# Kernel tuning notes

Hardware: AMD Instinct MI355X
Metric: run time of the kernel (lower is better)

Reference implementation:

```python
import jax, jax.numpy as jnp
import numpy as np

N = 200_000        # nodes
E = 2_000_000      # edges (before self loops)
D = 128            # emb_dim
L = 5              # num_layer
NUM_ATOM = 120     # num_atom_type
NUM_CHI = 3        # num_chirality_tag
NUM_BOND = 6       # num_bond_type
NUM_DIR = 3        # num_bond_direction
EPS = 1e-5


def setup_inputs() -> dict:
    key = jax.random.key(0)
    ks = jax.random.split(key, 12)
    s = 0.1
    return {
        "x": jax.random.randint(ks[0], (N, 2), 0, 3, dtype=jnp.int64) if jax.config.jax_enable_x64 else jax.random.randint(ks[0], (N, 2), 0, 3, dtype=jnp.int32),
        "edge_index": jax.random.randint(ks[1], (2, E), 0, N, dtype=jnp.int32),
        "edge_attr": jax.random.randint(ks[2], (E, 2), 0, 3, dtype=jnp.int32),
        "x_emb1": jax.random.normal(ks[3], (NUM_ATOM, D), jnp.float32) * s,
        "x_emb2": jax.random.normal(ks[4], (NUM_CHI, D), jnp.float32) * s,
        "edge_emb1": jax.random.normal(ks[5], (L, NUM_BOND, D), jnp.float32) * s,
        "edge_emb2": jax.random.normal(ks[6], (L, NUM_DIR, D), jnp.float32) * s,
        "w1": jax.random.normal(ks[7], (L, D, 2 * D), jnp.float32) * s,
        "b1": jnp.zeros((L, 2 * D), jnp.float32),
        "w2": jax.random.normal(ks[8], (L, 2 * D, D), jnp.float32) * s,
        "b2": jnp.zeros((L, D), jnp.float32),
        "bn_gamma": jnp.ones((L, D), jnp.float32),
        "bn_beta": jnp.zeros((L, D), jnp.float32),
    }


def reference(x, edge_index, edge_attr, x_emb1, x_emb2, edge_emb1, edge_emb2,
              w1, b1, w2, b2, bn_gamma, bn_beta):
    # node features: atom-type emb + chirality emb
    h = x_emb1[x[:, 0]] + x_emb2[x[:, 1]]                     # [N, D]

    # add self loops; self-loop edge_attr = [4, 0]
    loop = jnp.arange(N, dtype=edge_index.dtype)
    src = jnp.concatenate([edge_index[0], loop])              # [E+N]
    dst = jnp.concatenate([edge_index[1], loop])              # [E+N]
    ea0 = jnp.concatenate([edge_attr[:, 0], jnp.full((N,), 4, edge_attr.dtype)])
    ea1 = jnp.concatenate([edge_attr[:, 1], jnp.zeros((N,), edge_attr.dtype)])

    for l in range(L):
        e_emb = edge_emb1[l][ea0] + edge_emb2[l][ea1]         # [E+N, D]
        msg = h[src] + e_emb                                  # gather + add
        agg = jax.ops.segment_sum(msg, dst, num_segments=N)   # scatter-add
        hid = jax.nn.relu(agg @ w1[l] + b1[l])                # [N, 2D]
        hn = hid @ w2[l] + b2[l]                              # [N, D]
        # BatchNorm1d (training mode, biased variance)
        mean = hn.mean(axis=0)
        var = jnp.mean((hn - mean) ** 2, axis=0)
        hn = bn_gamma[l] * (hn - mean) * jax.lax.rsqrt(var + EPS) + bn_beta[l]
        if l < L - 1:
            hn = jax.nn.relu(hn)
        h = hn
    return h
```

## Files before the change

### kernel.cpp

```cpp
#include <hip/hip_runtime.h>

#define NN 200000
#define NPAD 200192
#define NE 2000000
#define DD 128
#define EPSF 1e-5f

typedef short short4v __attribute__((ext_vector_type(4)));
typedef short short8v __attribute__((ext_vector_type(8)));
typedef float f32x4 __attribute__((ext_vector_type(4)));
typedef unsigned long long u64;

__device__ __forceinline__ ushort f2bf(float f) {
  uint u = __float_as_uint(f);
  uint r = u + 0x7fff + ((u >> 16) & 1);
  return (ushort)(r >> 16);
}
__device__ __forceinline__ float bf2f(ushort u) { return __uint_as_float(((uint)u) << 16); }
__device__ __forceinline__ float bflo(uint v) { return __uint_as_float(v << 16); }
__device__ __forceinline__ float bfhi(uint v) { return __uint_as_float(v & 0xffff0000u); }
__device__ __forceinline__ uint packbf(float a, float b) {
  return (uint)f2bf(a) | ((uint)f2bf(b) << 16);
}

__device__ __forceinline__ short8v ldfrag(const ushort* p) {
  short4v lo = *(const short4v*)p;
  short4v hi = *(const short4v*)(p + 16);
  short8v r;
  r[0] = lo[0]; r[1] = lo[1]; r[2] = lo[2]; r[3] = lo[3];
  r[4] = hi[0]; r[5] = hi[1]; r[6] = hi[2]; r[7] = hi[3];
  return r;
}

__global__ __launch_bounds__(256) void k_init(const int* __restrict__ x,
    const float* __restrict__ e1, const float* __restrict__ e2,
    uint* __restrict__ h) {
  int t = blockIdx.x * 256 + threadIdx.x;
  if (t >= NN * 64) return;
  int node = t >> 6, cp = (t & 63) << 1;
  int a = x[2 * node], b = x[2 * node + 1];
  float2 va = *(const float2*)(e1 + (size_t)a * DD + cp);
  float2 vb = *(const float2*)(e2 + (size_t)b * DD + cp);
  h[t] = packbf(va.x + vb.x, va.y + vb.y);
}

__global__ __launch_bounds__(256) void k_cvtw(const float* __restrict__ w,
    ushort* __restrict__ wt, int K, int Nc) {
  int t = blockIdx.x * 256 + threadIdx.x;
  if (t >= 5 * K * Nc) return;
  int per = K * Nc;
  int l = t / per, r0 = t % per;
  int j = r0 & 7, lane = (r0 >> 3) & 63, idx = r0 >> 9;
  int KB = K >> 5;
  int kb = idx % KB, ct = idx / KB;
  int lr = lane & 15, qq = lane >> 4;
  int n = ct * 16 + lr;
  int k = kb * 32 + qq * 4 + (j & 3) + ((j >> 2) << 4);
  wt[t] = f2bf(w[(size_t)l * per + (size_t)k * Nc + n]);
}

__global__ __launch_bounds__(256) void k_hist(const int* __restrict__ ei,
    const int* __restrict__ ea, u64* __restrict__ hist) {
  int e = blockIdx.x * 256 + threadIdx.x;
  if (e >= NE) return;
  int d = ei[NE + e];
  int a0 = ea[2 * e];
  int a1 = ea[2 * e + 1];
  u64 v = (1ull << (a0 * 10)) | (1ull << (30 + a1 * 10));
  atomicAdd(&hist[d], v);
}

__global__ __launch_bounds__(256) void k_scan1(const u64* __restrict__ hist,
    int* __restrict__ off, int* __restrict__ bsum) {
  __shared__ int sh[256];
  int i = blockIdx.x * 256 + threadIdx.x;
  int v = 0;
  if (i < NN) {
    u64 hv = hist[i];
    v = (int)((hv & 1023) + ((hv >> 10) & 1023) + ((hv >> 20) & 1023));
  }
  sh[threadIdx.x] = v;
  __syncthreads();
  for (int d = 1; d < 256; d <<= 1) {
    int xv = 0;
    if (threadIdx.x >= d) xv = sh[threadIdx.x - d];
    __syncthreads();
    if (threadIdx.x >= d) sh[threadIdx.x] += xv;
    __syncthreads();
  }
  if (i < NN) off[i] = sh[threadIdx.x] - v;
  if (threadIdx.x == 255) bsum[blockIdx.x] = sh[255];
}

__global__ __launch_bounds__(1024) void k_scan2(const int* __restrict__ bsum,
    int* __restrict__ boff, int nb) {
  __shared__ int sh[1024];
  int t = threadIdx.x;
  int v = (t < nb) ? bsum[t] : 0;
  sh[t] = v;
  __syncthreads();
  for (int d = 1; d < 1024; d <<= 1) {
    int xv = 0;
    if (t >= d) xv = sh[t - d];
    __syncthreads();
    if (t >= d) sh[t] += xv;
    __syncthreads();
  }
  if (t < nb) boff[t] = sh[t] - v;
}

__global__ __launch_bounds__(256) void k_scan3(int* __restrict__ off,
    const int* __restrict__ boff, int* __restrict__ cursor) {
  int i = blockIdx.x * 256 + threadIdx.x;
  if (i < NN) {
    int o = off[i] + boff[i >> 8];
    off[i] = o;
    cursor[i] = o;
  }
  if (i == 0) off[NN] = NE;
}

__global__ __launch_bounds__(256) void k_scatter(const int* __restrict__ ei,
    int* __restrict__ cursor, int* __restrict__ csr_src) {
  int e = blockIdx.x * 256 + threadIdx.x;
  if (e >= NE) return;
  int d = ei[NE + e];
  int p = atomicAdd(&cursor[d], 1);
  csr_src[p] = ei[e];
}

__global__ __launch_bounds__(256) void k_agg(const uint* __restrict__ h,
    uint* __restrict__ agghi, uint* __restrict__ agglo,
    const int* __restrict__ off, const int* __restrict__ src,
    const u64* __restrict__ hist,
    const float* __restrict__ E1, const float* __restrict__ E2) {
  int lane = threadIdx.x & 63;
  int node = blockIdx.x * 4 + (threadIdx.x >> 6);
  int qq = lane >> 4;
  int c = lane & 15;
  float a[8];
#pragma unroll
  for (int j = 0; j < 8; ++j) a[j] = 0.f;
  int beg = off[node], end = off[node + 1];
  int deg = end - beg;
  for (int base = 0; base < deg; base += 64) {
    int nrem = min(deg - base, 64);
    int myidx = 0;
    if (lane < nrem) myidx = src[beg + base + lane];
    int niter = (nrem + 3) >> 2;
    for (int m = 0; m < niter; m += 2) {
      int slot0 = qq + 4 * m;
      int slot1 = slot0 + 4;
      int s0 = __shfl(myidx, min(slot0, nrem - 1));
      int s1 = __shfl(myidx, min(slot1, nrem - 1));
      uint4 v0 = *(const uint4*)(h + (size_t)s0 * 64 + c * 4);
      if (slot0 < nrem) {
        a[0] += bflo(v0.x); a[1] += bfhi(v0.x);
        a[2] += bflo(v0.y); a[3] += bfhi(v0.y);
        a[4] += bflo(v0.z); a[5] += bfhi(v0.z);
        a[6] += bflo(v0.w); a[7] += bfhi(v0.w);
      }
      if (m + 1 < niter) {
        uint4 v1 = *(const uint4*)(h + (size_t)s1 * 64 + c * 4);
        if (slot1 < nrem) {
          a[0] += bflo(v1.x); a[1] += bfhi(v1.x);
          a[2] += bflo(v1.y); a[3] += bfhi(v1.y);
          a[4] += bflo(v1.z); a[5] += bfhi(v1.z);
          a[6] += bflo(v1.w); a[7] += bfhi(v1.w);
        }
      }
    }
  }
#pragma unroll
  for (int j = 0; j < 8; ++j) {
    a[j] += __shfl_xor(a[j], 16);
    a[j] += __shfl_xor(a[j], 32);
  }
  if (lane < 16) {
    uint4 sv = *(const uint4*)(h + (size_t)node * 64 + c * 4);
    a[0] += bflo(sv.x); a[1] += bfhi(sv.x);
    a[2] += bflo(sv.y); a[3] += bfhi(sv.y);
    a[4] += bflo(sv.z); a[5] += bfhi(sv.z);
    a[6] += bflo(sv.w); a[7] += bfhi(sv.w);
    u64 hv = hist[node];
    float cnt[7] = {
      (float)(int)(hv & 1023),
      (float)(int)((hv >> 10) & 1023),
      (float)(int)((hv >> 20) & 1023),
      1.f,
      (float)(int)((hv >> 30) & 1023) + 1.f,
      (float)(int)((hv >> 40) & 1023),
      (float)(int)((hv >> 50) & 1023)
    };
    const float* rows[7] = {E1, E1 + DD, E1 + 2 * DD, E1 + 4 * DD,
                            E2, E2 + DD, E2 + 2 * DD};
#pragma unroll
    for (int q = 0; q < 7; ++q) {
      f32x4 e0 = *(const f32x4*)(rows[q] + c * 8);
      f32x4 e1v = *(const f32x4*)(rows[q] + c * 8 + 4);
#pragma unroll
      for (int j = 0; j < 4; ++j) { a[j] += cnt[q] * e0[j]; a[4 + j] += cnt[q] * e1v[j]; }
    }
    uint4 hi4, lo4;
    {
      ushort hA, hB;
      hA = f2bf(a[0]); hB = f2bf(a[1]);
      hi4.x = (uint)hA | ((uint)hB << 16);
      lo4.x = (uint)f2bf(a[0] - bf2f(hA)) | ((uint)f2bf(a[1] - bf2f(hB)) << 16);
      hA = f2bf(a[2]); hB = f2bf(a[3]);
      hi4.y = (uint)hA | ((uint)hB << 16);
      lo4.y = (uint)f2bf(a[2] - bf2f(hA)) | ((uint)f2bf(a[3] - bf2f(hB)) << 16);
      hA = f2bf(a[4]); hB = f2bf(a[5]);
      hi4.z = (uint)hA | ((uint)hB << 16);
      lo4.z = (uint)f2bf(a[4] - bf2f(hA)) | ((uint)f2bf(a[5] - bf2f(hB)) << 16);
      hA = f2bf(a[6]); hB = f2bf(a[7]);
      hi4.w = (uint)hA | ((uint)hB << 16);
      lo4.w = (uint)f2bf(a[6] - bf2f(hA)) | ((uint)f2bf(a[7] - bf2f(hB)) << 16);
    }
    *(uint4*)(agghi + (size_t)node * 64 + c * 4) = hi4;
    *(uint4*)(agglo + (size_t)node * 64 + c * 4) = lo4;
  }
}

__global__ __launch_bounds__(512, 1) void k_mlp(
    const ushort* __restrict__ agghi, const ushort* __restrict__ agglo,
    const ushort* __restrict__ w1,
    const float* __restrict__ b1,
    const ushort* __restrict__ w2,
    const float* __restrict__ b2, float* __restrict__ hn,
    float* __restrict__ bnsums) {
  __shared__ uint4 smem4[8192];
  __shared__ float sstat[256];
  const ushort* sw1 = (const ushort*)smem4;
  const ushort* sw2 = (const ushort*)(smem4 + 4096);
  int t = threadIdx.x;
  int lane = t & 63;
  int wid = t >> 6;
  int nb = blockIdx.x * 256 + wid * 32;
  int lr = lane & 15, qq = lane >> 4;

  if (t < 256) sstat[t] = 0.f;

  short8v afh[2][4], afl[2][4];
#pragma unroll
  for (int g = 0; g < 2; ++g) {
    const ushort* ph = agghi + (size_t)(nb + g * 16 + lr) * 128 + qq * 4;
    const ushort* pl = agglo + (size_t)(nb + g * 16 + lr) * 128 + qq * 4;
#pragma unroll
    for (int kb = 0; kb < 4; ++kb) {
      afh[g][kb] = ldfrag(ph + kb * 32);
      afl[g][kb] = ldfrag(pl + kb * 32);
    }
  }

  {
    const uint4* g1 = (const uint4*)w1;
    const uint4* g2 = (const uint4*)w2;
#pragma unroll
    for (int i = 0; i < 8; ++i) smem4[i * 512 + t] = g1[i * 512 + t];
#pragma unroll
    for (int i = 0; i < 8; ++i) smem4[4096 + i * 512 + t] = g2[i * 512 + t];
  }
  __syncthreads();

  f32x4 acc2[2][8];
#pragma unroll
  for (int g = 0; g < 2; ++g)
#pragma unroll
    for (int ct = 0; ct < 8; ++ct) acc2[g][ct] = (f32x4){0.f, 0.f, 0.f, 0.f};

#pragma unroll
  for (int ph = 0; ph < 4; ++ph) {
    f32x4 acc1[2][4];
#pragma unroll
    for (int g = 0; g < 2; ++g)
#pragma unroll
      for (int ct = 0; ct < 4; ++ct) acc1[g][ct] = (f32x4){0.f, 0.f, 0.f, 0.f};
#pragma unroll
    for (int ct = 0; ct < 4; ++ct) {
      int gct = ph * 4 + ct;
#pragma unroll
      for (int kb = 0; kb < 4; ++kb) {
        short8v wf = *(const short8v*)(sw1 + ((gct * 4 + kb) * 64 + lane) * 8);
        acc1[0][ct] = __builtin_amdgcn_mfma_f32_16x16x32_bf16(wf, afh[0][kb], acc1[0][ct], 0, 0, 0);
        acc1[0][ct] = __builtin_amdgcn_mfma_f32_16x16x32_bf16(wf, afl[0][kb], acc1[0][ct], 0, 0, 0);
        acc1[1][ct] = __builtin_amdgcn_mfma_f32_16x16x32_bf16(wf, afh[1][kb], acc1[1][ct], 0, 0, 0);
        acc1[1][ct] = __builtin_amdgcn_mfma_f32_16x16x32_bf16(wf, afl[1][kb], acc1[1][ct], 0, 0, 0);
      }
    }
    short8v hfh[2][2], hfl[2][2];
#pragma unroll
    for (int i = 0; i < 2; ++i) {
      f32x4 ba = *(const f32x4*)(b1 + (ph * 4 + 2 * i) * 16 + qq * 4);
      f32x4 bb = *(const f32x4*)(b1 + (ph * 4 + 2 * i + 1) * 16 + qq * 4);
#pragma unroll
      for (int g = 0; g < 2; ++g) {
        short8v hh, hl;
#pragma unroll
        for (int r = 0; r < 4; ++r) {
          float va = fmaxf(acc1[g][2 * i][r] + ba[r], 0.f);
          float vb = fmaxf(acc1[g][2 * i + 1][r] + bb[r], 0.f);
          ushort ha = f2bf(va), hb = f2bf(vb);
          hh[r] = (short)ha; hh[4 + r] = (short)hb;
          hl[r] = (short)f2bf(va - bf2f(ha));
          hl[4 + r] = (short)f2bf(vb - bf2f(hb));
        }
        hfh[g][i] = hh; hfl[g][i] = hl;
      }
    }
#pragma unroll
    for (int ct = 0; ct < 8; ++ct) {
#pragma unroll
      for (int i = 0; i < 2; ++i) {
        int kb2 = ph * 2 + i;
        short8v wf = *(const short8v*)(sw2 + ((ct * 8 + kb2) * 64 + lane) * 8);
        acc2[0][ct] = __builtin_amdgcn_mfma_f32_16x16x32_bf16(wf, hfh[0][i], acc2[0][ct], 0, 0, 0);
        acc2[0][ct] = __builtin_amdgcn_mfma_f32_16x16x32_bf16(wf, hfl[0][i], acc2[0][ct], 0, 0, 0);
        acc2[1][ct] = __builtin_amdgcn_mfma_f32_16x16x32_bf16(wf, hfh[1][i], acc2[1][ct], 0, 0, 0);
        acc2[1][ct] = __builtin_amdgcn_mfma_f32_16x16x32_bf16(wf, hfl[1][i], acc2[1][ct], 0, 0, 0);
      }
    }
  }

  int n0 = nb + lr, n1 = nb + 16 + lr;
  float m0 = (n0 < NN) ? 1.f : 0.f;
  float m1 = (n1 < NN) ? 1.f : 0.f;
#pragma unroll
  for (int ct = 0; ct < 8; ++ct) {
    f32x4 bb = *(const f32x4*)(b2 + ct * 16 + qq * 4);
    f32x4 o0, o1;
#pragma unroll
    for (int r = 0; r < 4; ++r) {
      o0[r] = acc2[0][ct][r] + bb[r];
      o1[r] = acc2[1][ct][r] + bb[r];
    }
#pragma unroll
    for (int r = 0; r < 4; ++r) {
      float s = m0 * o0[r] + m1 * o1[r];
      float q = m0 * o0[r] * o0[r] + m1 * o1[r] * o1[r];
      s += __shfl_xor(s, 1); q += __shfl_xor(q, 1);
      s += __shfl_xor(s, 2); q += __shfl_xor(q, 2);
      s += __shfl_xor(s, 4); q += __shfl_xor(q, 4);
      s += __shfl_xor(s, 8); q += __shfl_xor(q, 8);
      if (lr == 0) {
        int col = ct * 16 + qq * 4 + r;
        atomicAdd(&sstat[col], s);
        atomicAdd(&sstat[128 + col], q);
      }
    }
    if (n0 < NN) *(f32x4*)(hn + (size_t)n0 * DD + ct * 16 + qq * 4) = o0;
    if (n1 < NN) *(f32x4*)(hn + (size_t)n1 * DD + ct * 16 + qq * 4) = o1;
  }
  __syncthreads();
  if (t < 256) atomicAdd(&bnsums[t], sstat[t]);
}

__global__ __launch_bounds__(256) void k_bnapply(const float* __restrict__ hn,
    const float* __restrict__ sums, const float* __restrict__ gamma,
    const float* __restrict__ beta, uint* __restrict__ hout,
    float* __restrict__ fout, int final_layer) {
  int t = blockIdx.x * 256 + threadIdx.x;
  if (t >= NN * 64) return;
  int node = t >> 6, cp = (t & 63) << 1;
  float2 v = *(const float2*)(hn + (size_t)node * DD + cp);
  float r[2] = {v.x, v.y};
#pragma unroll
  for (int j = 0; j < 2; ++j) {
    int col = cp + j;
    float mean = sums[col] * (1.f / NN);
    float var = sums[128 + col] * (1.f / NN) - mean * mean;
    float scale = gamma[col] * rsqrtf(var + EPSF);
    r[j] = (r[j] - mean) * scale + beta[col];
  }
  if (final_layer) {
    *(float2*)(fout + (size_t)node * DD + cp) = make_float2(r[0], r[1]);
  } else {
    hout[t] = packbf(fmaxf(r[0], 0.f), fmaxf(r[1], 0.f));
  }
}

extern "C" void kernel_launch(void* const* d_in, const int* in_sizes, int n_in,
                              void* d_out, int out_size, void* d_ws, size_t ws_size,
                              hipStream_t stream) {
  const int* x    = (const int*)d_in[0];
  const int* ei   = (const int*)d_in[1];
  const int* ea   = (const int*)d_in[2];
  const float* xe1 = (const float*)d_in[3];
  const float* xe2 = (const float*)d_in[4];
  const float* ee1 = (const float*)d_in[5];
  const float* ee2 = (const float*)d_in[6];
  const float* w1  = (const float*)d_in[7];
  const float* b1  = (const float*)d_in[8];
  const float* w2  = (const float*)d_in[9];
  const float* b2  = (const float*)d_in[10];
  const float* gam = (const float*)d_in[11];
  const float* bet = (const float*)d_in[12];
  float* out = (float*)d_out;

  char* p = (char*)d_ws;
  auto alloc = [&](size_t bytes) {
    char* r = p;
    p += (bytes + 255) & ~(size_t)255;
    return r;
  };
  uint* h      = (uint*)alloc((size_t)NN * 64 * 4);
  uint* agghi  = (uint*)alloc((size_t)NPAD * 64 * 4);
  uint* agglo  = (uint*)alloc((size_t)NPAD * 64 * 4);
  float* hn    = (float*)alloc((size_t)NPAD * DD * 4);
  ushort* w1t  = (ushort*)alloc((size_t)5 * 128 * 256 * 2);
  ushort* w2t  = (ushort*)alloc((size_t)5 * 256 * 128 * 2);
  u64* hist    = (u64*)alloc((size_t)NN * 8);
  int* csroff  = (int*)alloc((size_t)(NN + 1) * 4);
  int* cursor  = (int*)alloc((size_t)NN * 4);
  int* csrsrc  = (int*)alloc((size_t)NE * 4);
  int* bsum    = (int*)alloc(4096);
  int* boff    = (int*)alloc(4096);
  float* bnsums = (float*)alloc(5 * 1024);

  const int nscan = (NN + 255) / 256;

  hipMemsetAsync(hist, 0, (size_t)NN * 8, stream);
  hipMemsetAsync(bnsums, 0, 5 * 1024, stream);

  k_cvtw<<<(5 * 128 * 256 + 255) / 256, 256, 0, stream>>>(w1, w1t, 128, 256);
  k_cvtw<<<(5 * 256 * 128 + 255) / 256, 256, 0, stream>>>(w2, w2t, 256, 128);
  k_init<<<(NN * 64 + 255) / 256, 256, 0, stream>>>(x, xe1, xe2, h);
  k_hist<<<(NE + 255) / 256, 256, 0, stream>>>(ei, ea, hist);
  k_scan1<<<nscan, 256, 0, stream>>>(hist, csroff, bsum);
  k_scan2<<<1, 1024, 0, stream>>>(bsum, boff, nscan);
  k_scan3<<<nscan, 256, 0, stream>>>(csroff, boff, cursor);
  k_scatter<<<(NE + 255) / 256, 256, 0, stream>>>(ei, cursor, csrsrc);

  for (int l = 0; l < 5; ++l) {
    k_agg<<<NN / 4, 256, 0, stream>>>(h, agghi, agglo, csroff, csrsrc, hist,
                                      ee1 + (size_t)l * 6 * DD,
                                      ee2 + (size_t)l * 3 * DD);
    k_mlp<<<NPAD / 256, 512, 0, stream>>>((const ushort*)agghi, (const ushort*)agglo,
                                          w1t + (size_t)l * 128 * 256,
                                          b1 + (size_t)l * 256,
                                          w2t + (size_t)l * 256 * 128,
                                          b2 + (size_t)l * DD, hn,
                                          bnsums + (size_t)l * 256);
    k_bnapply<<<(NN * 64 + 255) / 256, 256, 0, stream>>>(
        hn, bnsums + (size_t)l * 256, gam + (size_t)l * DD, bet + (size_t)l * DD,
        h, out, l == 4 ? 1 : 0);
  }
}
```

Baseline: 1.766 ms.

## Privatize degree histogram, unroll gather by four, and double MLP block size

The histogram atomics are spread over 8 private copies selected by block index, which the scan kernel sums and stores as a merged histogram. The goal is less atomic contention on destination nodes. The aggregation loop now issues four neighbor row loads per iteration instead of two, for more memory-level parallelism. The MLP kernel runs 1024-thread blocks over 512 rows, halving the number of times the weights are staged into shared memory per layer, at the cost of a larger memset and padded buffers.

Measured after the change: 2.629 ms. 1.49x slower.

```diff
diff --git a/kernel.cpp b/kernel.cpp
--- a/kernel.cpp
+++ b/kernel.cpp
@@ -1,7 +1,7 @@
 #include <hip/hip_runtime.h>
 
 #define NN 200000
-#define NPAD 200192
+#define NPAD 200704
 #define NE 2000000
 #define DD 128
 #define EPSF 1e-5f
@@ -60,24 +60,27 @@
 }
 
 __global__ __launch_bounds__(256) void k_hist(const int* __restrict__ ei,
-    const int* __restrict__ ea, u64* __restrict__ hist) {
+    const int* __restrict__ ea, u64* __restrict__ hist8) {
   int e = blockIdx.x * 256 + threadIdx.x;
   if (e >= NE) return;
   int d = ei[NE + e];
   int a0 = ea[2 * e];
   int a1 = ea[2 * e + 1];
   u64 v = (1ull << (a0 * 10)) | (1ull << (30 + a1 * 10));
-  atomicAdd(&hist[d], v);
-}
-
-__global__ __launch_bounds__(256) void k_scan1(const u64* __restrict__ hist,
-    int* __restrict__ off, int* __restrict__ bsum) {
+  atomicAdd(&hist8[(size_t)(blockIdx.x & 7) * NN + d], v);
+}
+
+__global__ __launch_bounds__(256) void k_scan1(const u64* __restrict__ hist8,
+    u64* __restrict__ histsum, int* __restrict__ off, int* __restrict__ bsum) {
   __shared__ int sh[256];
   int i = blockIdx.x * 256 + threadIdx.x;
   int v = 0;
   if (i < NN) {
-    u64 hv = hist[i];
-    v = (int)((hv & 1023) + ((hv >> 10) & 1023) + ((hv >> 20) & 1023));
+    u64 s = 0;
+#pragma unroll
+    for (int cc = 0; cc < 8; ++cc) s += hist8[(size_t)cc * NN + i];
+    histsum[i] = s;
+    v = (int)((s & 1023) + ((s >> 10) & 1023) + ((s >> 20) & 1023));
   }
   sh[threadIdx.x] = v;
   __syncthreads();
@@ -148,13 +151,15 @@
     int myidx = 0;
     if (lane < nrem) myidx = src[beg + base + lane];
     int niter = (nrem + 3) >> 2;
-    for (int m = 0; m < niter; m += 2) {
-      int slot0 = qq + 4 * m;
-      int slot1 = slot0 + 4;
-      int s0 = __shfl(myidx, min(slot0, nrem - 1));
-      int s1 = __shfl(myidx, min(slot1, nrem - 1));
+    for (int m = 0; m < niter; m += 4) {
+      int sl0 = qq + 4 * m;
+      int sl1 = sl0 + 4, sl2 = sl0 + 8, sl3 = sl0 + 12;
+      int s0 = __shfl(myidx, min(sl0, nrem - 1));
+      int s1 = __shfl(myidx, min(sl1, nrem - 1));
+      int s2 = __shfl(myidx, min(sl2, nrem - 1));
+      int s3 = __shfl(myidx, min(sl3, nrem - 1));
       uint4 v0 = *(const uint4*)(h + (size_t)s0 * 64 + c * 4);
-      if (slot0 < nrem) {
+      if (sl0 < nrem) {
         a[0] += bflo(v0.x); a[1] += bfhi(v0.x);
         a[2] += bflo(v0.y); a[3] += bfhi(v0.y);
         a[4] += bflo(v0.z); a[5] += bfhi(v0.z);
@@ -162,11 +167,29 @@
       }
       if (m + 1 < niter) {
         uint4 v1 = *(const uint4*)(h + (size_t)s1 * 64 + c * 4);
-        if (slot1 < nrem) {
+        if (sl1 < nrem) {
           a[0] += bflo(v1.x); a[1] += bfhi(v1.x);
           a[2] += bflo(v1.y); a[3] += bfhi(v1.y);
           a[4] += bflo(v1.z); a[5] += bfhi(v1.z);
           a[6] += bflo(v1.w); a[7] += bfhi(v1.w);
+        }
+      }
+      if (m + 2 < niter) {
+        uint4 v2 = *(const uint4*)(h + (size_t)s2 * 64 + c * 4);
+        if (sl2 < nrem) {
+          a[0] += bflo(v2.x); a[1] += bfhi(v2.x);
+          a[2] += bflo(v2.y); a[3] += bfhi(v2.y);
+          a[4] += bflo(v2.z); a[5] += bfhi(v2.z);
+          a[6] += bflo(v2.w); a[7] += bfhi(v2.w);
+        }
+      }
+      if (m + 3 < niter) {
+        uint4 v3 = *(const uint4*)(h + (size_t)s3 * 64 + c * 4);
+        if (sl3 < nrem) {
+          a[0] += bflo(v3.x); a[1] += bfhi(v3.x);
+          a[2] += bflo(v3.y); a[3] += bfhi(v3.y);
+          a[4] += bflo(v3.z); a[5] += bfhi(v3.z);
+          a[6] += bflo(v3.w); a[7] += bfhi(v3.w);
         }
       }
     }
@@ -222,7 +245,7 @@
   }
 }
 
-__global__ __launch_bounds__(512, 1) void k_mlp(
+__global__ __launch_bounds__(1024, 1) void k_mlp(
     const ushort* __restrict__ agghi, const ushort* __restrict__ agglo,
     const ushort* __restrict__ w1,
     const float* __restrict__ b1,
@@ -236,7 +259,7 @@
   int t = threadIdx.x;
   int lane = t & 63;
   int wid = t >> 6;
-  int nb = blockIdx.x * 256 + wid * 32;
+  int nb = blockIdx.x * 512 + wid * 32;
   int lr = lane & 15, qq = lane >> 4;
 
   if (t < 256) sstat[t] = 0.f;
@@ -257,9 +280,9 @@
     const uint4* g1 = (const uint4*)w1;
     const uint4* g2 = (const uint4*)w2;
 #pragma unroll
-    for (int i = 0; i < 8; ++i) smem4[i * 512 + t] = g1[i * 512 + t];
-#pragma unroll
-    for (int i = 0; i < 8; ++i) smem4[4096 + i * 512 + t] = g2[i * 512 + t];
+    for (int i = 0; i < 4; ++i) smem4[i * 1024 + t] = g1[i * 1024 + t];
+#pragma unroll
+    for (int i = 0; i < 4; ++i) smem4[4096 + i * 1024 + t] = g2[i * 1024 + t];
   }
   __syncthreads();
 
@@ -409,7 +432,8 @@
   float* hn    = (float*)alloc((size_t)NPAD * DD * 4);
   ushort* w1t  = (ushort*)alloc((size_t)5 * 128 * 256 * 2);
   ushort* w2t  = (ushort*)alloc((size_t)5 * 256 * 128 * 2);
-  u64* hist    = (u64*)alloc((size_t)NN * 8);
+  u64* hist8   = (u64*)alloc((size_t)8 * NN * 8);
+  u64* histsum = (u64*)alloc((size_t)NN * 8);
   int* csroff  = (int*)alloc((size_t)(NN + 1) * 4);
   int* cursor  = (int*)alloc((size_t)NN * 4);
   int* csrsrc  = (int*)alloc((size_t)NE * 4);
@@ -419,28 +443,28 @@
 
   const int nscan = (NN + 255) / 256;
 
-  hipMemsetAsync(hist, 0, (size_t)NN * 8, stream);
+  hipMemsetAsync(hist8, 0, (size_t)8 * NN * 8, stream);
   hipMemsetAsync(bnsums, 0, 5 * 1024, stream);
 
   k_cvtw<<<(5 * 128 * 256 + 255) / 256, 256, 0, stream>>>(w1, w1t, 128, 256);
   k_cvtw<<<(5 * 256 * 128 + 255) / 256, 256, 0, stream>>>(w2, w2t, 256, 128);
   k_init<<<(NN * 64 + 255) / 256, 256, 0, stream>>>(x, xe1, xe2, h);
-  k_hist<<<(NE + 255) / 256, 256, 0, stream>>>(ei, ea, hist);
-  k_scan1<<<nscan, 256, 0, stream>>>(hist, csroff, bsum);
+  k_hist<<<(NE + 255) / 256, 256, 0, stream>>>(ei, ea, hist8);
+  k_scan1<<<nscan, 256, 0, stream>>>(hist8, histsum, csroff, bsum);
   k_scan2<<<1, 1024, 0, stream>>>(bsum, boff, nscan);
   k_scan3<<<nscan, 256, 0, stream>>>(csroff, boff, cursor);
   k_scatter<<<(NE + 255) / 256, 256, 0, stream>>>(ei, cursor, csrsrc);
 
   for (int l = 0; l < 5; ++l) {
-    k_agg<<<NN / 4, 256, 0, stream>>>(h, agghi, agglo, csroff, csrsrc, hist,
+    k_agg<<<NN / 4, 256, 0, stream>>>(h, agghi, agglo, csroff, csrsrc, histsum,
                                       ee1 + (size_t)l * 6 * DD,
                                       ee2 + (size_t)l * 3 * DD);
-    k_mlp<<<NPAD / 256, 512, 0, stream>>>((const ushort*)agghi, (const ushort*)agglo,
-                                          w1t + (size_t)l * 128 * 256,
-                                          b1 + (size_t)l * 256,
-                                          w2t + (size_t)l * 256 * 128,
-                                          b2 + (size_t)l * DD, hn,
-                                          bnsums + (size_t)l * 256);
+    k_mlp<<<NPAD / 512, 1024, 0, stream>>>((const ushort*)agghi, (const ushort*)agglo,
+                                           w1t + (size_t)l * 128 * 256,
+                                           b1 + (size_t)l * 256,
+                                           w2t + (size_t)l * 256 * 128,
+                                           b2 + (size_t)l * DD, hn,
+                                           bnsums + (size_t)l * 256);
     k_bnapply<<<(NN * 64 + 255) / 256, 256, 0, stream>>>(
         hn, bnsums + (size_t)l * 256, gam + (size_t)l * DD, bet + (size_t)l * DD,
         h, out, l == 4 ? 1 : 0);
```
